# Performance work log

Measured on AMD Instinct MI355X. Metric: run time of the kernel, lower is better.

## Reference

```python
import jax, jax.numpy as jnp
import numpy as np

N_NODES = 100000
N_EDGES = 3200000
IN_CH = 128
HID = 64
OUT_CH = 40


def setup_inputs() -> dict:
    key = jax.random.key(0)
    ks = jax.random.split(key, 12)
    x = jax.random.normal(ks[0], (N_NODES, IN_CH), dtype=jnp.float32)
    edge_index = jax.random.randint(ks[1], (2, N_EDGES), 0, N_NODES, dtype=jnp.int64)
    def lin(k, fan_in, fan_out):
        bound = 1.0 / np.sqrt(fan_in)
        kw, kb = jax.random.split(k)
        W = jax.random.uniform(kw, (fan_in, fan_out), minval=-bound, maxval=bound, dtype=jnp.float32)
        b = jax.random.uniform(kb, (fan_out,), minval=-bound, maxval=bound, dtype=jnp.float32)
        return W, b
    W1, b1 = lin(ks[2], IN_CH, HID)   # nn1 layer 1
    W2, b2 = lin(ks[3], HID, HID)     # nn1 layer 2
    W3, b3 = lin(ks[4], HID, HID)     # nn2 layer 1
    W4, b4 = lin(ks[5], HID, HID)     # nn2 layer 2
    Wf, bf = lin(ks[6], HID, OUT_CH)  # final fc
    return {"x": x, "edge_index": edge_index,
            "W1": W1, "b1": b1, "W2": W2, "b2": b2,
            "W3": W3, "b3": b3, "W4": W4, "b4": b4,
            "Wf": Wf, "bf": bf}


def _gin_conv(x, src, dst, W_a, b_a, W_b, b_b):
    # GINConv (eps=0): out = MLP(x + sum_{j->i} x_j)
    agg = jax.ops.segment_sum(x[src], dst, num_segments=x.shape[0])
    h = x + agg
    h = jax.nn.relu(h @ W_a + b_a)
    return h @ W_b + b_b


def reference(x, edge_index, W1, b1, W2, b2, W3, b3, W4, b4, Wf, bf):
    src, dst = edge_index[0], edge_index[1]
    h = _gin_conv(x, src, dst, W1, b1, W2, b2)
    h = jax.nn.relu(h)  # dropout is identity at eval
    h = _gin_conv(h, src, dst, W3, b3, W4, b4)
    h = jax.nn.relu(h)
    logits = h @ Wf + bf
    return jax.nn.log_softmax(logits, axis=1)
```

## Files before the change

### kernel.cpp

```cpp
#include <hip/hip_runtime.h>
#include <math.h>

#define N_NODES_C 100000
#define N_EDGES_C 3200000
#define NB 782
#define BNODES 128
#define LDS_CAP 6144
#define CHUNK 16384
#define NBLK 196

typedef unsigned short u16;

__device__ __forceinline__ float bf2f(u16 u) {
    unsigned int t = ((unsigned int)u) << 16;
    return __uint_as_float(t);
}
__device__ __forceinline__ u16 f2bf(float f) {
    unsigned int x = __float_as_uint(f);
    x += 0x7fffu + ((x >> 16) & 1u);
    return (u16)(x >> 16);
}


__global__ __launch_bounds__(256) void passA_hist_kernel(const int* __restrict__ dst,
                                                         int* __restrict__ cnt, int n_edges) {
    __shared__ int h[NB];
    for (int i = threadIdx.x; i < NB; i += 256) h[i] = 0;
    __syncthreads();
    const int blk = blockIdx.x;
    const int end = min((blk + 1) * CHUNK, n_edges);
    for (int e = blk * CHUNK + threadIdx.x; e < end; e += 256)
        atomicAdd(&h[dst[e] >> 7], 1);
    __syncthreads();
    for (int i = threadIdx.x; i < NB; i += 256) cnt[i * NBLK + blk] = h[i];
}

__global__ __launch_bounds__(256) void scan_chunks_kernel(int* __restrict__ a, int n, int* __restrict__ bsums) {
    __shared__ int s[256];
    const int tid = threadIdx.x;
    int base = blockIdx.x * 1024 + tid * 4;
    int v[4];
#pragma unroll
    for (int i = 0; i < 4; ++i) v[i] = (base + i < n) ? a[base + i] : 0;
    int tsum = v[0] + v[1] + v[2] + v[3];
    s[tid] = tsum;
    __syncthreads();
    for (int off = 1; off < 256; off <<= 1) {
        int t = (tid >= off) ? s[tid - off] : 0;
        __syncthreads();
        s[tid] += t;
        __syncthreads();
    }
    int run = s[tid] - tsum;
#pragma unroll
    for (int i = 0; i < 4; ++i) {
        run += v[i];
        if (base + i < n) a[base + i] = run;
    }
    if (tid == 255) bsums[blockIdx.x] = s[255];
}

__global__ __launch_bounds__(256) void scan_sums_kernel(int* __restrict__ bsums, int nb) {
    __shared__ int s[256];
    const int tid = threadIdx.x;
    int v = (tid < nb) ? bsums[tid] : 0;
    s[tid] = v;
    __syncthreads();
    for (int off = 1; off < 256; off <<= 1) {
        int t = (tid >= off) ? s[tid - off] : 0;
        __syncthreads();
        s[tid] += t;
        __syncthreads();
    }
    if (tid < nb) bsums[tid] = s[tid] - v;
}

__global__ __launch_bounds__(256) void scan_add_kernel(int* __restrict__ a, int n, const int* __restrict__ bsums) {
    int base = blockIdx.x * 1024 + threadIdx.x * 4;
    int add = bsums[blockIdx.x];
#pragma unroll
    for (int i = 0; i < 4; ++i)
        if (base + i < n) a[base + i] += add;
}

__global__ __launch_bounds__(1024) void boffs_kernel(const int* __restrict__ incl,
                                                     int* __restrict__ boffs,
                                                     int* __restrict__ offs) {
    const int b = threadIdx.x;
    if (b < NB) boffs[b] = b ? incl[b * NBLK - 1] : 0;
    if (b == 0) {
        int total = incl[NB * NBLK - 1];
        boffs[NB] = total;
        offs[N_NODES_C] = total;
    }
}

__global__ __launch_bounds__(256) void passB_sort_kernel(const int* __restrict__ src,
                                                         const int* __restrict__ dst,
                                                         const int* __restrict__ incl,
                                                         unsigned int* __restrict__ stage,
                                                         int n_edges) {
    __shared__ unsigned int sdst[CHUNK];
    __shared__ unsigned int spack[CHUNK];
    __shared__ int hist[NB];
    __shared__ int lcur[NB];
    __shared__ int tsum[256];
    const int blk = blockIdx.x, tid = threadIdx.x;
    const int e0 = blk * CHUNK;
    const int cntE = min(CHUNK, n_edges - e0);

    for (int b = tid; b < NB; b += 256) hist[b] = 0;
    __syncthreads();

    if (cntE == CHUNK) {
        for (int i = tid * 4; i < CHUNK; i += 1024) {
            int4 d4 = *(const int4*)&dst[e0 + i];
            sdst[i + 0] = (unsigned)d4.x; sdst[i + 1] = (unsigned)d4.y;
            sdst[i + 2] = (unsigned)d4.z; sdst[i + 3] = (unsigned)d4.w;
            atomicAdd(&hist[d4.x >> 7], 1); atomicAdd(&hist[d4.y >> 7], 1);
            atomicAdd(&hist[d4.z >> 7], 1); atomicAdd(&hist[d4.w >> 7], 1);
        }
    } else {
        for (int i = tid; i < cntE; i += 256) {
            int d = dst[e0 + i];
            sdst[i] = (unsigned)d;
            atomicAdd(&hist[d >> 7], 1);
        }
    }
    __syncthreads();

    {
        int loc[4];
        const int bi = tid * 4;
        int s = 0;
#pragma unroll
        for (int k = 0; k < 4; ++k) {
            int idx = bi + k;
            loc[k] = (idx < NB) ? hist[idx] : 0;
            s += loc[k];
        }
        tsum[tid] = s;
        __syncthreads();
        for (int off = 1; off < 256; off <<= 1) {
            int t = (tid >= off) ? tsum[tid - off] : 0;
            __syncthreads();
            tsum[tid] += t;
            __syncthreads();
        }
        int run = tsum[tid] - s;
#pragma unroll
        for (int k = 0; k < 4; ++k) {
            int idx = bi + k;
            if (idx < NB) {
                int h = loc[k];
                hist[idx] = run;
                lcur[idx] = run;
                run += h;
            }
        }
    }
    __syncthreads();

    if (cntE == CHUNK) {
        for (int i = tid * 4; i < CHUNK; i += 1024) {
            int4 s4 = *(const int4*)&src[e0 + i];
            unsigned int d; int p;
            d = sdst[i + 0]; p = atomicAdd(&lcur[d >> 7], 1); spack[p] = (unsigned)s4.x | ((d & 127u) << 17);
            d = sdst[i + 1]; p = atomicAdd(&lcur[d >> 7], 1); spack[p] = (unsigned)s4.y | ((d & 127u) << 17);
            d = sdst[i + 2]; p = atomicAdd(&lcur[d >> 7], 1); spack[p] = (unsigned)s4.z | ((d & 127u) << 17);
            d = sdst[i + 3]; p = atomicAdd(&lcur[d >> 7], 1); spack[p] = (unsigned)s4.w | ((d & 127u) << 17);
        }
    } else {
        for (int i = tid; i < cntE; i += 256) {
            unsigned int d = sdst[i];
            int p = atomicAdd(&lcur[d >> 7], 1);
            spack[p] = (unsigned)src[e0 + i] | ((d & 127u) << 17);
        }
    }
    __syncthreads();

    for (int b = tid; b < NB; b += 256) {
        int l0 = hist[b];
        int l1 = (b + 1 < NB) ? hist[b + 1] : cntE;
        int idx = b * NBLK + blk;
        int g0 = idx ? incl[idx - 1] : 0;
        for (int j = l0; j < l1; ++j) stage[g0 + (j - l0)] = spack[j];
    }
}

__global__ __launch_bounds__(256) void bucket_finalize_kernel(const unsigned int* __restrict__ stage,
                                                              const int* __restrict__ boffs,
                                                              int* __restrict__ offs,
                                                              int* __restrict__ srcs) {
    __shared__ int hist[BNODES];
    __shared__ int excl[BNODES];
    __shared__ int curs[BNODES];
    __shared__ int sbuf[LDS_CAP];
    const int b = blockIdx.x, tid = threadIdx.x;
    const int base = boffs[b];
    const int count = boffs[b + 1] - base;
    const int n0 = b * BNODES;
    for (int i = tid; i < BNODES; i += 256) hist[i] = 0;
    __syncthreads();
    for (int i = tid; i < count; i += 256) {
        unsigned int w = stage[base + i];
        atomicAdd(&hist[w >> 17], 1);
    }
    __syncthreads();
    if (tid < BNODES) excl[tid] = hist[tid];
    __syncthreads();
    for (int off = 1; off < BNODES; off <<= 1) {
        int t = 0;
        if (tid < BNODES && tid >= off) t = excl[tid - off];
        __syncthreads();
        if (tid < BNODES) excl[tid] += t;
        __syncthreads();
    }
    if (tid < BNODES) {
        int ex = excl[tid] - hist[tid];
        int n = n0 + tid;
        if (n < N_NODES_C) offs[n] = base + ex;
        curs[tid] = ex;
    }
    __syncthreads();
    if (count <= LDS_CAP) {
        for (int i = tid; i < count; i += 256) {
            unsigned int w = stage[base + i];
            int p = atomicAdd(&curs[w >> 17], 1);
            sbuf[p] = (int)(w & 0x1FFFFu);
        }
        __syncthreads();
        for (int i = tid; i < count; i += 256) srcs[base + i] = sbuf[i];
    } else {
        for (int i = tid; i < count; i += 256) {
            unsigned int w = stage[base + i];
            int p = atomicAdd(&curs[w >> 17], 1);
            srcs[base + p] = (int)(w & 0x1FFFFu);
        }
    }
}


__global__ __launch_bounds__(256) void gather64v_kernel(const u16* __restrict__ feat,
                                                        const int* __restrict__ offs,
                                                        const int* __restrict__ srcs,
                                                        const float* __restrict__ bias,
                                                        float* __restrict__ out, int n_nodes) {
    const int wave = threadIdx.x >> 6;
    const int lane = threadIdx.x & 63;
    const int grp  = lane >> 4;
    const int cl   = lane & 15;
    const int n = blockIdx.x * 4 + wave;
    if (n >= n_nodes) return;

    float a0 = 0.f, a1 = 0.f, a2 = 0.f, a3 = 0.f;
    if (grp == 0) {
        ushort4 v = *(const ushort4*)&feat[(size_t)n * 64 + cl * 4];
        a0 = bf2f(v.x); a1 = bf2f(v.y); a2 = bf2f(v.z); a3 = bf2f(v.w);
    }
    const int s0 = offs[n], s1 = offs[n + 1];
    int i = s0;
    for (; i + 16 <= s1; i += 16) {
        int r0 = srcs[i + grp];
        int r1 = srcs[i + 4 + grp];
        int r2 = srcs[i + 8 + grp];
        int r3 = srcs[i + 12 + grp];
        ushort4 v0 = *(const ushort4*)&feat[(size_t)r0 * 64 + cl * 4];
        ushort4 v1 = *(const ushort4*)&feat[(size_t)r1 * 64 + cl * 4];
        ushort4 v2 = *(const ushort4*)&feat[(size_t)r2 * 64 + cl * 4];
        ushort4 v3 = *(const ushort4*)&feat[(size_t)r3 * 64 + cl * 4];
        a0 += bf2f(v0.x); a1 += bf2f(v0.y); a2 += bf2f(v0.z); a3 += bf2f(v0.w);
        a0 += bf2f(v1.x); a1 += bf2f(v1.y); a2 += bf2f(v1.z); a3 += bf2f(v1.w);
        a0 += bf2f(v2.x); a1 += bf2f(v2.y); a2 += bf2f(v2.z); a3 += bf2f(v2.w);
        a0 += bf2f(v3.x); a1 += bf2f(v3.y); a2 += bf2f(v3.z); a3 += bf2f(v3.w);
    }
    for (; i + 4 <= s1; i += 4) {
        int r = srcs[i + grp];
        ushort4 v = *(const ushort4*)&feat[(size_t)r * 64 + cl * 4];
        a0 += bf2f(v.x); a1 += bf2f(v.y); a2 += bf2f(v.z); a3 += bf2f(v.w);
    }
    if (i + grp < s1) {
        int r = srcs[i + grp];
        ushort4 v = *(const ushort4*)&feat[(size_t)r * 64 + cl * 4];
        a0 += bf2f(v.x); a1 += bf2f(v.y); a2 += bf2f(v.z); a3 += bf2f(v.w);
    }
    a0 += __shfl_xor(a0, 16); a1 += __shfl_xor(a1, 16);
    a2 += __shfl_xor(a2, 16); a3 += __shfl_xor(a3, 16);
    a0 += __shfl_xor(a0, 32); a1 += __shfl_xor(a1, 32);
    a2 += __shfl_xor(a2, 32); a3 += __shfl_xor(a3, 32);
    if (lane < 16) {
        float4 b = *(const float4*)&bias[cl * 4];
        float4 o;
        o.x = fmaxf(a0 + b.x, 0.f);
        o.y = fmaxf(a1 + b.y, 0.f);
        o.z = fmaxf(a2 + b.z, 0.f);
        o.w = fmaxf(a3 + b.w, 0.f);
        *(float4*)&out[(size_t)n * 64 + cl * 4] = o;
    }
}

#define GIN_STEP(ai, i)                                                                               \
    acc[i][0] += ai.x * w0.x; acc[i][1] += ai.x * w0.y; acc[i][2] += ai.x * w0.z; acc[i][3] += ai.x * w0.w; \
    acc[i][0] += ai.y * w1.x; acc[i][1] += ai.y * w1.y; acc[i][2] += ai.y * w1.z; acc[i][3] += ai.y * w1.w; \
    acc[i][0] += ai.z * w2.x; acc[i][1] += ai.z * w2.y; acc[i][2] += ai.z * w2.z; acc[i][3] += ai.z * w2.w; \
    acc[i][0] += ai.w * w3.x; acc[i][1] += ai.w * w3.y; acc[i][2] += ai.w * w3.z; acc[i][3] += ai.w * w3.w;


__global__ __launch_bounds__(256) void dense128_kernel(const float* __restrict__ in,
                                                       const float* __restrict__ W,
                                                       u16* __restrict__ out, int n_nodes) {
    __shared__ float sW[128 * 64];
    const int tid = threadIdx.x;
    for (int i = tid; i < 128 * 16; i += 256) ((float4*)sW)[i] = ((const float4*)W)[i];
    __syncthreads();
    const int tj = tid & 15, tn = tid >> 4;
    const int j0 = tj * 4, n0 = blockIdx.x * 64 + tn * 4;
    const int r0 = min(n0 + 0, n_nodes - 1), r1 = min(n0 + 1, n_nodes - 1);
    const int r2 = min(n0 + 2, n_nodes - 1), r3 = min(n0 + 3, n_nodes - 1);
    float acc[4][4];
#pragma unroll
    for (int i = 0; i < 4; ++i)
#pragma unroll
        for (int j = 0; j < 4; ++j) acc[i][j] = 0.f;
#pragma unroll 4
    for (int k = 0; k < 128; k += 4) {
        float4 a0 = *(const float4*)&in[(size_t)r0 * 128 + k];
        float4 a1 = *(const float4*)&in[(size_t)r1 * 128 + k];
        float4 a2 = *(const float4*)&in[(size_t)r2 * 128 + k];
        float4 a3 = *(const float4*)&in[(size_t)r3 * 128 + k];
        float4 w0 = *(const float4*)&sW[(k + 0) * 64 + j0];
        float4 w1 = *(const float4*)&sW[(k + 1) * 64 + j0];
        float4 w2 = *(const float4*)&sW[(k + 2) * 64 + j0];
        float4 w3 = *(const float4*)&sW[(k + 3) * 64 + j0];
        GIN_STEP(a0, 0) GIN_STEP(a1, 1) GIN_STEP(a2, 2) GIN_STEP(a3, 3)
    }
#pragma unroll
    for (int i = 0; i < 4; ++i) {
        int n = n0 + i;
        if (n < n_nodes) {
            ushort4 o;
            o.x = f2bf(acc[i][0]); o.y = f2bf(acc[i][1]);
            o.z = f2bf(acc[i][2]); o.w = f2bf(acc[i][3]);
            *(ushort4*)&out[(size_t)n * 64 + j0] = o;
        }
    }
}


__global__ __launch_bounds__(256) void fused_w2w3_kernel(const float* __restrict__ in,
                                                         const float* __restrict__ W2,
                                                         const float* __restrict__ b2,
                                                         const float* __restrict__ W3,
                                                         u16* __restrict__ out, int n_nodes) {
    __shared__ float sW2[64 * 64];
    __shared__ float sW3[64 * 64];
    __shared__ float sT[64][68];
    const int tid = threadIdx.x;
    for (int i = tid; i < 64 * 16; i += 256) {
        ((float4*)sW2)[i] = ((const float4*)W2)[i];
        ((float4*)sW3)[i] = ((const float4*)W3)[i];
    }
    __syncthreads();
    const int tj = tid & 15, tn = tid >> 4;
    const int j0 = tj * 4, n0l = tn * 4;
    const int base = blockIdx.x * 64;
    const int r0 = min(base + n0l + 0, n_nodes - 1), r1 = min(base + n0l + 1, n_nodes - 1);
    const int r2 = min(base + n0l + 2, n_nodes - 1), r3 = min(base + n0l + 3, n_nodes - 1);
    float acc[4][4];
#pragma unroll
    for (int i = 0; i < 4; ++i)
#pragma unroll
        for (int j = 0; j < 4; ++j) acc[i][j] = b2[j0 + j];
#pragma unroll 4
    for (int k = 0; k < 64; k += 4) {
        float4 a0 = *(const float4*)&in[(size_t)r0 * 64 + k];
        float4 a1 = *(const float4*)&in[(size_t)r1 * 64 + k];
        float4 a2 = *(const float4*)&in[(size_t)r2 * 64 + k];
        float4 a3 = *(const float4*)&in[(size_t)r3 * 64 + k];
        float4 w0 = *(const float4*)&sW2[(k + 0) * 64 + j0];
        float4 w1 = *(const float4*)&sW2[(k + 1) * 64 + j0];
        float4 w2 = *(const float4*)&sW2[(k + 2) * 64 + j0];
        float4 w3 = *(const float4*)&sW2[(k + 3) * 64 + j0];
        GIN_STEP(a0, 0) GIN_STEP(a1, 1) GIN_STEP(a2, 2) GIN_STEP(a3, 3)
    }
#pragma unroll
    for (int i = 0; i < 4; ++i) {
        float4 t;
        t.x = fmaxf(acc[i][0], 0.f); t.y = fmaxf(acc[i][1], 0.f);
        t.z = fmaxf(acc[i][2], 0.f); t.w = fmaxf(acc[i][3], 0.f);
        *(float4*)&sT[n0l + i][j0] = t;
    }
    __syncthreads();
#pragma unroll
    for (int i = 0; i < 4; ++i)
#pragma unroll
        for (int j = 0; j < 4; ++j) acc[i][j] = 0.f;
#pragma unroll 4
    for (int k = 0; k < 64; k += 4) {
        float4 a0 = *(const float4*)&sT[n0l + 0][k];
        float4 a1 = *(const float4*)&sT[n0l + 1][k];
        float4 a2 = *(const float4*)&sT[n0l + 2][k];
        float4 a3 = *(const float4*)&sT[n0l + 3][k];
        float4 w0 = *(const float4*)&sW3[(k + 0) * 64 + j0];
        float4 w1 = *(const float4*)&sW3[(k + 1) * 64 + j0];
        float4 w2 = *(const float4*)&sW3[(k + 2) * 64 + j0];
        float4 w3 = *(const float4*)&sW3[(k + 3) * 64 + j0];
        GIN_STEP(a0, 0) GIN_STEP(a1, 1) GIN_STEP(a2, 2) GIN_STEP(a3, 3)
    }
#pragma unroll
    for (int i = 0; i < 4; ++i) {
        int n = base + n0l + i;
        if (n < n_nodes) {
            ushort4 o;
            o.x = f2bf(acc[i][0]); o.y = f2bf(acc[i][1]);
            o.z = f2bf(acc[i][2]); o.w = f2bf(acc[i][3]);
            *(ushort4*)&out[(size_t)n * 64 + j0] = o;
        }
    }
}


__global__ __launch_bounds__(256) void fused_w4final_kernel(const float* __restrict__ in,
                                                            const float* __restrict__ W4,
                                                            const float* __restrict__ b4,
                                                            const float* __restrict__ Wf,
                                                            const float* __restrict__ bfin,
                                                            float* __restrict__ out, int n_nodes) {
    __shared__ float smem[11008];
    float* sW4 = smem;
    float* sWf = smem + 4096;
    float* sTf = smem + 6656;
    float* sLog = smem;
    const int tid = threadIdx.x;
    const int base = blockIdx.x * 64;
    for (int i = tid; i < 64 * 16; i += 256) ((float4*)sW4)[i] = ((const float4*)W4)[i];
    for (int i = tid; i < 64 * 10; i += 256) ((float4*)sWf)[i] = ((const float4*)Wf)[i];
    __syncthreads();
    {
        const int tj = tid & 15, tn = tid >> 4;
        const int j0 = tj * 4, n0l = tn * 4;
        const int r0 = min(base + n0l + 0, n_nodes - 1), r1 = min(base + n0l + 1, n_nodes - 1);
        const int r2 = min(base + n0l + 2, n_nodes - 1), r3 = min(base + n0l + 3, n_nodes - 1);
        float acc[4][4];
#pragma unroll
        for (int i = 0; i < 4; ++i)
#pragma unroll
            for (int j = 0; j < 4; ++j) acc[i][j] = b4[j0 + j];
#pragma unroll 4
        for (int k = 0; k < 64; k += 4) {
            float4 a0 = *(const float4*)&in[(size_t)r0 * 64 + k];
            float4 a1 = *(const float4*)&in[(size_t)r1 * 64 + k];
            float4 a2 = *(const float4*)&in[(size_t)r2 * 64 + k];
            float4 a3 = *(const float4*)&in[(size_t)r3 * 64 + k];
            float4 w0 = *(const float4*)&sW4[(k + 0) * 64 + j0];
            float4 w1 = *(const float4*)&sW4[(k + 1) * 64 + j0];
            float4 w2 = *(const float4*)&sW4[(k + 2) * 64 + j0];
            float4 w3 = *(const float4*)&sW4[(k + 3) * 64 + j0];
            GIN_STEP(a0, 0) GIN_STEP(a1, 1) GIN_STEP(a2, 2) GIN_STEP(a3, 3)
        }
#pragma unroll
        for (int i = 0; i < 4; ++i) {
            float4 t;
            t.x = fmaxf(acc[i][0], 0.f); t.y = fmaxf(acc[i][1], 0.f);
            t.z = fmaxf(acc[i][2], 0.f); t.w = fmaxf(acc[i][3], 0.f);
            *(float4*)&sTf[(n0l + i) * 68 + j0] = t;
        }
    }
    __syncthreads();
    if (tid < 160) {
        const int tj = tid % 10, tn = tid / 10;
        const int j0 = tj * 4, n0l = tn * 4;
        float acc[4][4];
#pragma unroll
        for (int i = 0; i < 4; ++i)
#pragma unroll
            for (int j = 0; j < 4; ++j) acc[i][j] = bfin[j0 + j];
#pragma unroll 4
        for (int k = 0; k < 64; k += 4) {
            float4 a0 = *(const float4*)&sTf[(n0l + 0) * 68 + k];
            float4 a1 = *(const float4*)&sTf[(n0l + 1) * 68 + k];
            float4 a2 = *(const float4*)&sTf[(n0l + 2) * 68 + k];
            float4 a3 = *(const float4*)&sTf[(n0l + 3) * 68 + k];
            float4 w0 = *(const float4*)&sWf[(k + 0) * 40 + j0];
            float4 w1 = *(const float4*)&sWf[(k + 1) * 40 + j0];
            float4 w2 = *(const float4*)&sWf[(k + 2) * 40 + j0];
            float4 w3 = *(const float4*)&sWf[(k + 3) * 40 + j0];
            GIN_STEP(a0, 0) GIN_STEP(a1, 1) GIN_STEP(a2, 2) GIN_STEP(a3, 3)
        }
#pragma unroll
        for (int i = 0; i < 4; ++i)
            *(float4*)&sLog[(n0l + i) * 40 + j0] = make_float4(acc[i][0], acc[i][1], acc[i][2], acc[i][3]);
    }
    __syncthreads();
    if (tid < 64) {
        const int nl = tid;
        const int n = base + nl;
        if (n < n_nodes) {
            float m = -1e30f;
            for (int j = 0; j < 40; ++j) m = fmaxf(m, sLog[nl * 40 + j]);
            float s = 0.f;
            for (int j = 0; j < 40; ++j) s += expf(sLog[nl * 40 + j] - m);
            float lse = m + logf(s);
            for (int j = 0; j < 40; j += 4) {
                float4 o;
                o.x = sLog[nl * 40 + j + 0] - lse;
                o.y = sLog[nl * 40 + j + 1] - lse;
                o.z = sLog[nl * 40 + j + 2] - lse;
                o.w = sLog[nl * 40 + j + 3] - lse;
                *(float4*)&out[(size_t)n * 40 + j] = o;
            }
        }
    }
}


extern "C" void kernel_launch(void* const* d_in, const int* in_sizes, int n_in,
                              void* d_out, int out_size, void* d_ws, size_t ws_size,
                              hipStream_t stream) {
    const float* x  = (const float*)d_in[0];
    const int*   ei = (const int*)d_in[1];
    const float* W1 = (const float*)d_in[2];
    const float* b1 = (const float*)d_in[3];
    const float* W2 = (const float*)d_in[4];
    const float* b2 = (const float*)d_in[5];
    const float* W3 = (const float*)d_in[6];
    const float* b3 = (const float*)d_in[7];
    const float* W4 = (const float*)d_in[8];
    const float* b4 = (const float*)d_in[9];
    const float* Wf = (const float*)d_in[10];
    const float* bf = (const float*)d_in[11];
    float* outp = (float*)d_out;

    const int N = N_NODES_C, E = N_EDGES_C;
    const int* srcp = ei;
    const int* dstp = ei + E;

    char* ws = (char*)d_ws;
    int*          offs  = (int*)(ws);
    int*          boffs = (int*)(ws + 400128);
    int*          bsums = (int*)(ws + 404352);
    int*          cnt   = (int*)(ws + 405376);
    unsigned int* stage = (unsigned int*)(ws + 1018624);
    int*          srcs  = (int*)(ws + 13818624);
    u16*          Ybf   = (u16*)(ws + 26618624);
    float*        F2    = (float*)(ws + 39418624);

    passA_hist_kernel<<<NBLK, 256, 0, stream>>>(dstp, cnt, E);
    const int n_scan = NB * NBLK;
    const int nblk_scan = (n_scan + 1023) / 1024;
    scan_chunks_kernel<<<nblk_scan, 256, 0, stream>>>(cnt, n_scan, bsums);
    scan_sums_kernel<<<1, 256, 0, stream>>>(bsums, nblk_scan);
    scan_add_kernel<<<nblk_scan, 256, 0, stream>>>(cnt, n_scan, bsums);
    boffs_kernel<<<1, 1024, 0, stream>>>(cnt, boffs, offs);
    passB_sort_kernel<<<NBLK, 256, 0, stream>>>(srcp, dstp, cnt, stage, E);
    bucket_finalize_kernel<<<NB, 256, 0, stream>>>(stage, boffs, offs, srcs);

    const int mlp_grid = (N + 63) / 64;
    const int gat_grid = (N + 3) / 4;

    dense128_kernel<<<mlp_grid, 256, 0, stream>>>(x, W1, Ybf, N);
    gather64v_kernel<<<gat_grid, 256, 0, stream>>>(Ybf, offs, srcs, b1, F2, N);
    fused_w2w3_kernel<<<mlp_grid, 256, 0, stream>>>(F2, W2, b2, W3, Ybf, N);

    gather64v_kernel<<<gat_grid, 256, 0, stream>>>(Ybf, offs, srcs, b3, F2, N);
    fused_w4final_kernel<<<mlp_grid, 256, 0, stream>>>(F2, W4, b4, Wf, bf, outp, N);
}
```

Measured before the change: 301.6 us.

## Halve sort chunk size, store gather output in bf16, unroll gather loop deeper

```diff
diff --git a/kernel.cpp b/kernel.cpp
--- a/kernel.cpp
+++ b/kernel.cpp
@@ -6,8 +6,8 @@
 #define NB 782
 #define BNODES 128
 #define LDS_CAP 6144
-#define CHUNK 16384
-#define NBLK 196
+#define CHUNK 8192
+#define NBLK 391
 
 typedef unsigned short u16;
 
@@ -28,9 +28,13 @@
     for (int i = threadIdx.x; i < NB; i += 256) h[i] = 0;
     __syncthreads();
     const int blk = blockIdx.x;
-    const int end = min((blk + 1) * CHUNK, n_edges);
-    for (int e = blk * CHUNK + threadIdx.x; e < end; e += 256)
-        atomicAdd(&h[dst[e] >> 7], 1);
+    const int e0 = blk * CHUNK;
+    const int cntE = min(CHUNK, n_edges - e0);
+    for (int i = threadIdx.x * 4; i < cntE; i += 1024) {
+        int4 d4 = *(const int4*)&dst[e0 + i];
+        atomicAdd(&h[d4.x >> 7], 1); atomicAdd(&h[d4.y >> 7], 1);
+        atomicAdd(&h[d4.z >> 7], 1); atomicAdd(&h[d4.w >> 7], 1);
+    }
     __syncthreads();
     for (int i = threadIdx.x; i < NB; i += 256) cnt[i * NBLK + blk] = h[i];
 }
@@ -60,13 +64,13 @@
     if (tid == 255) bsums[blockIdx.x] = s[255];
 }
 
-__global__ __launch_bounds__(256) void scan_sums_kernel(int* __restrict__ bsums, int nb) {
-    __shared__ int s[256];
+__global__ __launch_bounds__(512) void scan_sums_kernel(int* __restrict__ bsums, int nb) {
+    __shared__ int s[512];
     const int tid = threadIdx.x;
     int v = (tid < nb) ? bsums[tid] : 0;
     s[tid] = v;
     __syncthreads();
-    for (int off = 1; off < 256; off <<= 1) {
+    for (int off = 1; off < 512; off <<= 1) {
         int t = (tid >= off) ? s[tid - off] : 0;
         __syncthreads();
         s[tid] += t;
@@ -100,7 +104,6 @@
                                                          const int* __restrict__ incl,
                                                          unsigned int* __restrict__ stage,
                                                          int n_edges) {
-    __shared__ unsigned int sdst[CHUNK];
     __shared__ unsigned int spack[CHUNK];
     __shared__ int hist[NB];
     __shared__ int lcur[NB];
@@ -112,20 +115,10 @@
     for (int b = tid; b < NB; b += 256) hist[b] = 0;
     __syncthreads();
 
-    if (cntE == CHUNK) {
-        for (int i = tid * 4; i < CHUNK; i += 1024) {
-            int4 d4 = *(const int4*)&dst[e0 + i];
-            sdst[i + 0] = (unsigned)d4.x; sdst[i + 1] = (unsigned)d4.y;
-            sdst[i + 2] = (unsigned)d4.z; sdst[i + 3] = (unsigned)d4.w;
-            atomicAdd(&hist[d4.x >> 7], 1); atomicAdd(&hist[d4.y >> 7], 1);
-            atomicAdd(&hist[d4.z >> 7], 1); atomicAdd(&hist[d4.w >> 7], 1);
-        }
-    } else {
-        for (int i = tid; i < cntE; i += 256) {
-            int d = dst[e0 + i];
-            sdst[i] = (unsigned)d;
-            atomicAdd(&hist[d >> 7], 1);
-        }
+    for (int i = tid * 4; i < cntE; i += 1024) {
+        int4 d4 = *(const int4*)&dst[e0 + i];
+        atomicAdd(&hist[d4.x >> 7], 1); atomicAdd(&hist[d4.y >> 7], 1);
+        atomicAdd(&hist[d4.z >> 7], 1); atomicAdd(&hist[d4.w >> 7], 1);
     }
     __syncthreads();
 
@@ -161,21 +154,14 @@
     }
     __syncthreads();
 
-    if (cntE == CHUNK) {
-        for (int i = tid * 4; i < CHUNK; i += 1024) {
-            int4 s4 = *(const int4*)&src[e0 + i];
-            unsigned int d; int p;
-            d = sdst[i + 0]; p = atomicAdd(&lcur[d >> 7], 1); spack[p] = (unsigned)s4.x | ((d & 127u) << 17);
-            d = sdst[i + 1]; p = atomicAdd(&lcur[d >> 7], 1); spack[p] = (unsigned)s4.y | ((d & 127u) << 17);
-            d = sdst[i + 2]; p = atomicAdd(&lcur[d >> 7], 1); spack[p] = (unsigned)s4.z | ((d & 127u) << 17);
-            d = sdst[i + 3]; p = atomicAdd(&lcur[d >> 7], 1); spack[p] = (unsigned)s4.w | ((d & 127u) << 17);
-        }
-    } else {
-        for (int i = tid; i < cntE; i += 256) {
-            unsigned int d = sdst[i];
-            int p = atomicAdd(&lcur[d >> 7], 1);
-            spack[p] = (unsigned)src[e0 + i] | ((d & 127u) << 17);
-        }
+    for (int i = tid * 4; i < cntE; i += 1024) {
+        int4 d4 = *(const int4*)&dst[e0 + i];
+        int4 s4 = *(const int4*)&src[e0 + i];
+        int p;
+        p = atomicAdd(&lcur[d4.x >> 7], 1); spack[p] = (unsigned)s4.x | (((unsigned)d4.x & 127u) << 17);
+        p = atomicAdd(&lcur[d4.y >> 7], 1); spack[p] = (unsigned)s4.y | (((unsigned)d4.y & 127u) << 17);
+        p = atomicAdd(&lcur[d4.z >> 7], 1); spack[p] = (unsigned)s4.z | (((unsigned)d4.z & 127u) << 17);
+        p = atomicAdd(&lcur[d4.w >> 7], 1); spack[p] = (unsigned)s4.w | (((unsigned)d4.w & 127u) << 17);
     }
     __syncthreads();
 
@@ -245,7 +231,7 @@
                                                         const int* __restrict__ offs,
                                                         const int* __restrict__ srcs,
                                                         const float* __restrict__ bias,
-                                                        float* __restrict__ out, int n_nodes) {
+                                                        u16* __restrict__ out, int n_nodes) {
     const int wave = threadIdx.x >> 6;
     const int lane = threadIdx.x & 63;
     const int grp  = lane >> 4;
@@ -260,28 +246,34 @@
     }
     const int s0 = offs[n], s1 = offs[n + 1];
     int i = s0;
-    for (; i + 16 <= s1; i += 16) {
-        int r0 = srcs[i + grp];
-        int r1 = srcs[i + 4 + grp];
-        int r2 = srcs[i + 8 + grp];
-        int r3 = srcs[i + 12 + grp];
-        ushort4 v0 = *(const ushort4*)&feat[(size_t)r0 * 64 + cl * 4];
-        ushort4 v1 = *(const ushort4*)&feat[(size_t)r1 * 64 + cl * 4];
-        ushort4 v2 = *(const ushort4*)&feat[(size_t)r2 * 64 + cl * 4];
-        ushort4 v3 = *(const ushort4*)&feat[(size_t)r3 * 64 + cl * 4];
-        a0 += bf2f(v0.x); a1 += bf2f(v0.y); a2 += bf2f(v0.z); a3 += bf2f(v0.w);
-        a0 += bf2f(v1.x); a1 += bf2f(v1.y); a2 += bf2f(v1.z); a3 += bf2f(v1.w);
-        a0 += bf2f(v2.x); a1 += bf2f(v2.y); a2 += bf2f(v2.z); a3 += bf2f(v2.w);
-        a0 += bf2f(v3.x); a1 += bf2f(v3.y); a2 += bf2f(v3.z); a3 += bf2f(v3.w);
+    for (; i + 32 <= s1; i += 32) {
+        int r[8];
+#pragma unroll
+        for (int u = 0; u < 8; ++u) r[u] = srcs[i + u * 4 + grp];
+        ushort4 v[8];
+#pragma unroll
+        for (int u = 0; u < 8; ++u) v[u] = *(const ushort4*)&feat[(size_t)r[u] * 64 + cl * 4];
+#pragma unroll
+        for (int u = 0; u < 8; ++u) {
+            a0 += bf2f(v[u].x); a1 += bf2f(v[u].y); a2 += bf2f(v[u].z); a3 += bf2f(v[u].w);
+        }
+    }
+    for (; i + 8 <= s1; i += 8) {
+        int ra = srcs[i + grp];
+        int rb = srcs[i + 4 + grp];
+        ushort4 va = *(const ushort4*)&feat[(size_t)ra * 64 + cl * 4];
+        ushort4 vb = *(const ushort4*)&feat[(size_t)rb * 64 + cl * 4];
+        a0 += bf2f(va.x); a1 += bf2f(va.y); a2 += bf2f(va.z); a3 += bf2f(va.w);
+        a0 += bf2f(vb.x); a1 += bf2f(vb.y); a2 += bf2f(vb.z); a3 += bf2f(vb.w);
     }
     for (; i + 4 <= s1; i += 4) {
-        int r = srcs[i + grp];
-        ushort4 v = *(const ushort4*)&feat[(size_t)r * 64 + cl * 4];
+        int rr = srcs[i + grp];
+        ushort4 v = *(const ushort4*)&feat[(size_t)rr * 64 + cl * 4];
         a0 += bf2f(v.x); a1 += bf2f(v.y); a2 += bf2f(v.z); a3 += bf2f(v.w);
     }
     if (i + grp < s1) {
-        int r = srcs[i + grp];
-        ushort4 v = *(const ushort4*)&feat[(size_t)r * 64 + cl * 4];
+        int rr = srcs[i + grp];
+        ushort4 v = *(const ushort4*)&feat[(size_t)rr * 64 + cl * 4];
         a0 += bf2f(v.x); a1 += bf2f(v.y); a2 += bf2f(v.z); a3 += bf2f(v.w);
     }
     a0 += __shfl_xor(a0, 16); a1 += __shfl_xor(a1, 16);
@@ -290,12 +282,12 @@
     a2 += __shfl_xor(a2, 32); a3 += __shfl_xor(a3, 32);
     if (lane < 16) {
         float4 b = *(const float4*)&bias[cl * 4];
-        float4 o;
-        o.x = fmaxf(a0 + b.x, 0.f);
-        o.y = fmaxf(a1 + b.y, 0.f);
-        o.z = fmaxf(a2 + b.z, 0.f);
-        o.w = fmaxf(a3 + b.w, 0.f);
-        *(float4*)&out[(size_t)n * 64 + cl * 4] = o;
+        ushort4 o;
+        o.x = f2bf(fmaxf(a0 + b.x, 0.f));
+        o.y = f2bf(fmaxf(a1 + b.y, 0.f));
+        o.z = f2bf(fmaxf(a2 + b.z, 0.f));
+        o.w = f2bf(fmaxf(a3 + b.w, 0.f));
+        *(ushort4*)&out[(size_t)n * 64 + cl * 4] = o;
     }
 }
 
@@ -304,6 +296,8 @@
     acc[i][0] += ai.y * w1.x; acc[i][1] += ai.y * w1.y; acc[i][2] += ai.y * w1.z; acc[i][3] += ai.y * w1.w; \
     acc[i][0] += ai.z * w2.x; acc[i][1] += ai.z * w2.y; acc[i][2] += ai.z * w2.z; acc[i][3] += ai.z * w2.w; \
     acc[i][0] += ai.w * w3.x; acc[i][1] += ai.w * w3.y; acc[i][2] += ai.w * w3.z; acc[i][3] += ai.w * w3.w;
+
+#define BF4_TO_F4(u4) make_float4(bf2f(u4.x), bf2f(u4.y), bf2f(u4.z), bf2f(u4.w))
 
 
 __global__ __launch_bounds__(256) void dense128_kernel(const float* __restrict__ in,
@@ -347,7 +341,7 @@
 }
 
 
-__global__ __launch_bounds__(256) void fused_w2w3_kernel(const float* __restrict__ in,
+__global__ __launch_bounds__(256) void fused_w2w3_kernel(const u16* __restrict__ in,
                                                          const float* __restrict__ W2,
                                                          const float* __restrict__ b2,
                                                          const float* __restrict__ W3,
@@ -373,10 +367,14 @@
         for (int j = 0; j < 4; ++j) acc[i][j] = b2[j0 + j];
 #pragma unroll 4
     for (int k = 0; k < 64; k += 4) {
-        float4 a0 = *(const float4*)&in[(size_t)r0 * 64 + k];
-        float4 a1 = *(const float4*)&in[(size_t)r1 * 64 + k];
-        float4 a2 = *(const float4*)&in[(size_t)r2 * 64 + k];
-        float4 a3 = *(const float4*)&in[(size_t)r3 * 64 + k];
+        ushort4 u0 = *(const ushort4*)&in[(size_t)r0 * 64 + k];
+        ushort4 u1 = *(const ushort4*)&in[(size_t)r1 * 64 + k];
+        ushort4 u2 = *(const ushort4*)&in[(size_t)r2 * 64 + k];
+        ushort4 u3 = *(const ushort4*)&in[(size_t)r3 * 64 + k];
+        float4 a0 = BF4_TO_F4(u0);
+        float4 a1 = BF4_TO_F4(u1);
+        float4 a2 = BF4_TO_F4(u2);
+        float4 a3 = BF4_TO_F4(u3);
         float4 w0 = *(const float4*)&sW2[(k + 0) * 64 + j0];
         float4 w1 = *(const float4*)&sW2[(k + 1) * 64 + j0];
         float4 w2 = *(const float4*)&sW2[(k + 2) * 64 + j0];
@@ -420,7 +418,7 @@
 }
 
 
-__global__ __launch_bounds__(256) void fused_w4final_kernel(const float* __restrict__ in,
+__global__ __launch_bounds__(256) void fused_w4final_kernel(const u16* __restrict__ in,
                                                             const float* __restrict__ W4,
                                                             const float* __restrict__ b4,
                                                             const float* __restrict__ Wf,
@@ -448,10 +446,14 @@
             for (int j = 0; j < 4; ++j) acc[i][j] = b4[j0 + j];
 #pragma unroll 4
         for (int k = 0; k < 64; k += 4) {
-            float4 a0 = *(const float4*)&in[(size_t)r0 * 64 + k];
-            float4 a1 = *(const float4*)&in[(size_t)r1 * 64 + k];
-            float4 a2 = *(const float4*)&in[(size_t)r2 * 64 + k];
-            float4 a3 = *(const float4*)&in[(size_t)r3 * 64 + k];
+            ushort4 u0 = *(const ushort4*)&in[(size_t)r0 * 64 + k];
+            ushort4 u1 = *(const ushort4*)&in[(size_t)r1 * 64 + k];
+            ushort4 u2 = *(const ushort4*)&in[(size_t)r2 * 64 + k];
+            ushort4 u3 = *(const ushort4*)&in[(size_t)r3 * 64 + k];
+            float4 a0 = BF4_TO_F4(u0);
+            float4 a1 = BF4_TO_F4(u1);
+            float4 a2 = BF4_TO_F4(u2);
+            float4 a3 = BF4_TO_F4(u3);
             float4 w0 = *(const float4*)&sW4[(k + 0) * 64 + j0];
             float4 w1 = *(const float4*)&sW4[(k + 1) * 64 + j0];
             float4 w2 = *(const float4*)&sW4[(k + 2) * 64 + j0];
@@ -538,18 +540,18 @@
     char* ws = (char*)d_ws;
     int*          offs  = (int*)(ws);
     int*          boffs = (int*)(ws + 400128);
-    int*          bsums = (int*)(ws + 404352);
+    int*          bsums = (int*)(ws + 403328);
     int*          cnt   = (int*)(ws + 405376);
-    unsigned int* stage = (unsigned int*)(ws + 1018624);
-    int*          srcs  = (int*)(ws + 13818624);
-    u16*          Ybf   = (u16*)(ws + 26618624);
-    float*        F2    = (float*)(ws + 39418624);
+    unsigned int* stage = (unsigned int*)(ws + 1628672);
+    int*          srcs  = (int*)(ws + 14428672);
+    u16*          Ybf   = (u16*)(ws + 27228672);
+    u16*          F2bf  = (u16*)(ws + 40028672);
 
     passA_hist_kernel<<<NBLK, 256, 0, stream>>>(dstp, cnt, E);
     const int n_scan = NB * NBLK;
     const int nblk_scan = (n_scan + 1023) / 1024;
     scan_chunks_kernel<<<nblk_scan, 256, 0, stream>>>(cnt, n_scan, bsums);
-    scan_sums_kernel<<<1, 256, 0, stream>>>(bsums, nblk_scan);
+    scan_sums_kernel<<<1, 512, 0, stream>>>(bsums, nblk_scan);
     scan_add_kernel<<<nblk_scan, 256, 0, stream>>>(cnt, n_scan, bsums);
     boffs_kernel<<<1, 1024, 0, stream>>>(cnt, boffs, offs);
     passB_sort_kernel<<<NBLK, 256, 0, stream>>>(srcp, dstp, cnt, stage, E);
@@ -559,9 +561,9 @@
     const int gat_grid = (N + 3) / 4;
 
     dense128_kernel<<<mlp_grid, 256, 0, stream>>>(x, W1, Ybf, N);
-    gather64v_kernel<<<gat_grid, 256, 0, stream>>>(Ybf, offs, srcs, b1, F2, N);
-    fused_w2w3_kernel<<<mlp_grid, 256, 0, stream>>>(F2, W2, b2, W3, Ybf, N);
-
-    gather64v_kernel<<<gat_grid, 256, 0, stream>>>(Ybf, offs, srcs, b3, F2, N);
-    fused_w4final_kernel<<<mlp_grid, 256, 0, stream>>>(F2, W4, b4, Wf, bf, outp, N);
-}
+    gather64v_kernel<<<gat_grid, 256, 0, stream>>>(Ybf, offs, srcs, b1, F2bf, N);
+    fused_w2w3_kernel<<<mlp_grid, 256, 0, stream>>>(F2bf, W2, b2, W3, Ybf, N);
+
+    gather64v_kernel<<<gat_grid, 256, 0, stream>>>(Ybf, offs, srcs, b3, F2bf, N);
+    fused_w4final_kernel<<<mlp_grid, 256, 0, stream>>>(F2bf, W4, b4, Wf, bf, outp, N);
+}
```

Measured after the change: 289.1 us. -4.1%, faster.
